# Optimization experiments

Hardware: AMD Instinct MI355X
Metric: run time of the kernel (lower is better)

The kernel has to match this reference:

```python
import jax, jax.numpy as jnp
import numpy as np

B, N, M, D = 64, 197, 65, 768


def setup_inputs() -> dict:
    key = jax.random.key(0)
    k1, k2, k3 = jax.random.split(key, 3)
    image = jax.random.normal(k1, (B, N, D), dtype=jnp.float32)
    text = jax.random.normal(k2, (B, M, D), dtype=jnp.float32)
    pm = jax.random.randint(k3, (B, M), 0, 2).astype(jnp.int32)
    pm = pm.at[:, :2].set(0)  # CLS + first real token always valid
    logit_scale = jnp.ones((), dtype=jnp.float32)
    return {"image": image, "text": text, "padding_masks": pm, "logit_scale": logit_scale}


def _ce_with_diag_labels(logits):
    # F.cross_entropy(logits, arange(B)): mean of -log_softmax diag
    return -jnp.mean(jnp.diagonal(jax.nn.log_softmax(logits, axis=-1)))


def reference(image, text, padding_masks, logit_scale):
    # include_cls_token=False: original computes full [B,B,N,M] then slices
    # [:, :, 1:, 1:]; we compute the sliced tokens directly (same math).
    img = image[:, 1:, :]                   # [B, N-1, D]
    txt = text[:, 1:, :]                    # [B, M-1, D]
    pm = padding_masks[:, 1:].astype(bool)  # [B, M-1] True = padded

    # sim[i,j,n,m] = logit_scale * <img_i,n , txt_j,m>
    sim = logit_scale * jnp.einsum('ind,jmd->ijnm', img, txt)  # [B,B,N-1,M-1]

    # Original masks with NaN along mask of batch-row i (broadcast over j,n).
    # logits_per_image: nan_to_num(-inf) -> max over m -> mean over n
    sim_img = jnp.where(pm[:, None, None, :], -jnp.inf, sim)
    logits_per_image = jnp.mean(jnp.max(sim_img, axis=3), axis=2)  # [B,B]

    # logits_per_text: max over n (NaN cols stay NaN) -> nanmean over m.
    # Equivalent masked mean over valid m (mask constant along n).
    max_n = jnp.max(sim, axis=2)                         # [B,B,M-1]
    valid = ~pm                                          # [B,M-1]
    cnt = jnp.sum(valid, axis=1).astype(sim.dtype)       # [B]
    logits_per_text = jnp.sum(
        jnp.where(valid[:, None, :], max_n, 0.0), axis=2
    ) / cnt[:, None]                                     # [B,B]

    loss = 0.5 * (_ce_with_diag_labels(logits_per_image)
                  + _ce_with_diag_labels(logits_per_text))
    targets = jnp.arange(logits_per_image.shape[0], dtype=jnp.int32)
    return loss, logits_per_image, logits_per_text, targets
```

## Files before the change

### kernel.cpp

```cpp
#include <hip/hip_runtime.h>

typedef _Float16 half8 __attribute__((ext_vector_type(8)));
typedef float floatx4 __attribute__((ext_vector_type(4)));
typedef float float4v __attribute__((ext_vector_type(4)));

#define DIM   768
#define NROW  196
#define AUNITS (64 * 13 * 24 * 64)
#define TUNITS (64 * 4 * 24 * 64)
#define A_HALFS ((size_t)AUNITS * 8)
#define BJ_HALFS (24 * 4 * 64 * 8)

__device__ __forceinline__ void gl_lds16(const _Float16* g, _Float16* l) {
  __builtin_amdgcn_global_load_lds(
      (const __attribute__((address_space(1))) unsigned int*)g,
      (__attribute__((address_space(3))) unsigned int*)l, 16, 0, 0);
}

__global__ __launch_bounds__(256) void repack(const float* __restrict__ img,
                                              const float* __restrict__ txt,
                                              _Float16* __restrict__ Apk,
                                              _Float16* __restrict__ Bpk) {
  int gid = blockIdx.x * 256 + threadIdx.x;
  const float* src;
  _Float16* dst;
  if (gid < AUNITS) {
    int l = gid & 63, g = gid >> 6;
    int s = g % 24; g /= 24;
    int tau = g % 13; int i = g / 13;
    int n = tau * 16 + (l & 15); if (n > 195) n = 195;
    src = img + (size_t)i * 197 * 768 + (size_t)(n + 1) * 768 + s * 32 + (l >> 4) * 8;
    dst = Apk + (size_t)gid * 8;
  } else {
    int u = gid - AUNITS;
    int l = u & 63, g = u >> 6;
    int ct = g & 3; g >>= 2;
    int s = g % 24; int j = g / 24;
    int m = ct * 16 + (l & 15);
    src = txt + (size_t)j * 65 * 768 + (size_t)(m + 1) * 768 + s * 32 + (l >> 4) * 8;
    dst = Bpk + (size_t)u * 8;
  }
  float4v v0 = *(const float4v*)src;
  float4v v1 = *(const float4v*)(src + 4);
  half8 h;
  h[0] = (_Float16)v0[0]; h[1] = (_Float16)v0[1]; h[2] = (_Float16)v0[2]; h[3] = (_Float16)v0[3];
  h[4] = (_Float16)v1[0]; h[5] = (_Float16)v1[1]; h[6] = (_Float16)v1[2]; h[7] = (_Float16)v1[3];
  *(half8*)dst = h;
}

__global__ __launch_bounds__(256, 3) void sim_kernel(const _Float16* __restrict__ Apk,
                                                     const _Float16* __restrict__ Bpk,
                                                     const int* __restrict__ pm,
                                                     const float* __restrict__ ls,
                                                     float* __restrict__ lpi,
                                                     float* __restrict__ lpt) {
  __shared__ _Float16 Bsh[24576];
  __shared__ float colmaxLDS[4][64];
  __shared__ float t12buf[4][64];
  __shared__ float wsumLDS[4];

  const int j = blockIdx.x, i = blockIdx.y;
  const int tid = threadIdx.x;
  const int wave = tid >> 6, lane = tid & 63;
  const int r16 = lane & 15;
  const int lane8 = lane * 8;

  const _Float16* Ai = Apk + (size_t)i * 13 * 24 * 512;
  const _Float16* pA[4];
  pA[0] = Ai + (size_t)(wave)     * 24 * 512 + lane8;
  pA[1] = Ai + (size_t)(wave + 4) * 24 * 512 + lane8;
  pA[2] = Ai + (size_t)(wave + 8) * 24 * 512 + lane8;
  pA[3] = Ai + (size_t)12         * 24 * 512 + lane8;
  const _Float16* Bg = Bpk + (size_t)j * BJ_HALFS;

  half8 af[2][4];
#pragma unroll
  for (int t = 0; t < 4; ++t) {
    af[0][t] = *(const half8*)(pA[t]);
    af[1][t] = *(const half8*)(pA[t] + 512);
  }

  floatx4 acc[3][4];
  floatx4 acc12 = (floatx4){0.f, 0.f, 0.f, 0.f};
#pragma unroll
  for (int t = 0; t < 3; ++t)
#pragma unroll
    for (int cc = 0; cc < 4; ++cc)
      acc[t][cc] = (floatx4){0.f, 0.f, 0.f, 0.f};

  for (int h = 0; h < 2; ++h) {
    __syncthreads();
#pragma unroll
    for (int r = 0; r < 12; ++r) {
      int u = wave * 12 + r;
      gl_lds16(Bg + h * 24576 + u * 512 + lane8, Bsh + u * 512);
    }
    __syncthreads();

#pragma unroll
    for (int sc = 0; sc < 12; ++sc) {
      half8 bfr[4];
#pragma unroll
      for (int cc = 0; cc < 4; ++cc) {
        int ct = (wave + cc) & 3;
        bfr[cc] = *(const half8*)(Bsh + (sc * 4 + ct) * 512 + lane8);
      }
      half8 a0 = af[sc & 1][0], a1 = af[sc & 1][1], a2 = af[sc & 1][2], a3 = af[sc & 1][3];
      if (h == 0 || sc < 10) {
        int s2 = h * 12 + sc + 2;
#pragma unroll
        for (int t = 0; t < 4; ++t) af[sc & 1][t] = *(const half8*)(pA[t] + s2 * 512);
      }
#pragma unroll
      for (int cc = 0; cc < 4; ++cc) {
        acc[0][cc] = __builtin_amdgcn_mfma_f32_16x16x32_f16(a0, bfr[cc], acc[0][cc], 0, 0, 0);
        acc[1][cc] = __builtin_amdgcn_mfma_f32_16x16x32_f16(a1, bfr[cc], acc[1][cc], 0, 0, 0);
        acc[2][cc] = __builtin_amdgcn_mfma_f32_16x16x32_f16(a2, bfr[cc], acc[2][cc], 0, 0, 0);
      }
      acc12 = __builtin_amdgcn_mfma_f32_16x16x32_f16(a3, bfr[0], acc12, 0, 0, 0);
    }
  }

  const float sgl = ls[0];
  bool msk[4];
  int colc[4];
#pragma unroll
  for (int cc = 0; cc < 4; ++cc) {
    colc[cc] = ((wave + cc) & 3) * 16 + r16;
    msk[cc] = pm[i * 65 + 1 + colc[cc]] != 0;
  }

  float rowsum = 0.f;
#pragma unroll
  for (int t = 0; t < 3; ++t) {
#pragma unroll
    for (int r = 0; r < 4; ++r) {
      float rm = -__builtin_inff();
#pragma unroll
      for (int cc = 0; cc < 4; ++cc) {
        float v = acc[t][cc][r] * sgl;
        rm = fmaxf(rm, msk[cc] ? -__builtin_inff() : v);
      }
#pragma unroll
      for (int off = 1; off < 16; off <<= 1)
        rm = fmaxf(rm, __shfl_xor(rm, off, 64));
      rowsum += rm;
    }
  }
#pragma unroll
  for (int off = 1; off < 64; off <<= 1) rowsum += __shfl_xor(rowsum, off, 64);
  if (lane == 0) wsumLDS[wave] = rowsum;

#pragma unroll
  for (int cc = 0; cc < 4; ++cc) {
    float cm = -__builtin_inff();
#pragma unroll
    for (int t = 0; t < 3; ++t)
#pragma unroll
      for (int r = 0; r < 4; ++r)
        cm = fmaxf(cm, acc[t][cc][r] * sgl);
    cm = fmaxf(cm, __shfl_xor(cm, 16, 64));
    cm = fmaxf(cm, __shfl_xor(cm, 32, 64));
    if (lane < 16) colmaxLDS[wave][colc[cc]] = cm;
  }
  if (lane < 16) {
#pragma unroll
    for (int r = 0; r < 4; ++r) t12buf[r][wave * 16 + r16] = acc12[r] * sgl;
  }
  __syncthreads();

  if (tid < 64) {
    int col = tid;
    bool valid = pm[i * 65 + 1 + col] == 0;
    float t0 = t12buf[0][col], t1 = t12buf[1][col], t2 = t12buf[2][col], t3 = t12buf[3][col];
    float v = fmaxf(fmaxf(colmaxLDS[0][col], colmaxLDS[1][col]),
                    fmaxf(colmaxLDS[2][col], colmaxLDS[3][col]));
    v = fmaxf(v, fmaxf(fmaxf(t0, t1), fmaxf(t2, t3)));
    float contrib = valid ? v : 0.f;
    float cntv = valid ? 1.f : 0.f;
    float rs0 = valid ? t0 : -__builtin_inff();
    float rs1 = valid ? t1 : -__builtin_inff();
    float rs2 = valid ? t2 : -__builtin_inff();
    float rs3 = valid ? t3 : -__builtin_inff();
#pragma unroll
    for (int off = 1; off < 64; off <<= 1) {
      contrib += __shfl_xor(contrib, off, 64);
      cntv += __shfl_xor(cntv, off, 64);
      rs0 = fmaxf(rs0, __shfl_xor(rs0, off, 64));
      rs1 = fmaxf(rs1, __shfl_xor(rs1, off, 64));
      rs2 = fmaxf(rs2, __shfl_xor(rs2, off, 64));
      rs3 = fmaxf(rs3, __shfl_xor(rs3, off, 64));
    }
    if (tid == 0) {
      lpt[i * 64 + j] = contrib / cntv;
      float total = (wsumLDS[0] + wsumLDS[1] + wsumLDS[2] + wsumLDS[3]) * 0.0625f
                  + rs0 + rs1 + rs2 + rs3;
      lpi[i * 64 + j] = total / 196.f;
    }
  }
}

__global__ __launch_bounds__(64) void ce_kernel(float* __restrict__ out) {
  const int t = threadIdx.x;
  const float* lpi = out + 1;
  const float* lpt = out + 1 + 4096;

  float mx = -__builtin_inff();
  for (int jj = 0; jj < 64; ++jj) mx = fmaxf(mx, lpi[t * 64 + jj]);
  float se = 0.f;
  for (int jj = 0; jj < 64; ++jj) se += __expf(lpi[t * 64 + jj] - mx);
  float ci = (mx + __logf(se)) - lpi[t * 64 + t];

  float mx2 = -__builtin_inff();
  for (int jj = 0; jj < 64; ++jj) mx2 = fmaxf(mx2, lpt[t * 64 + jj]);
  float se2 = 0.f;
  for (int jj = 0; jj < 64; ++jj) se2 += __expf(lpt[t * 64 + jj] - mx2);
  float ct_ = (mx2 + __logf(se2)) - lpt[t * 64 + t];

  float v = ci + ct_;
#pragma unroll
  for (int off = 1; off < 64; off <<= 1) v += __shfl_xor(v, off, 64);
  if (t == 0) out[0] = 0.5f * v / 64.f;
  out[1 + 8192 + t] = (float)t;
}

extern "C" void kernel_launch(void* const* d_in, const int* in_sizes, int n_in,
                              void* d_out, int out_size, void* d_ws, size_t ws_size,
                              hipStream_t stream) {
  const float* image = (const float*)d_in[0];
  const float* text  = (const float*)d_in[1];
  const int*   pm    = (const int*)d_in[2];
  const float* ls    = (const float*)d_in[3];
  float* out = (float*)d_out;

  _Float16* Apk = (_Float16*)d_ws;
  _Float16* Bpk = Apk + A_HALFS;

  repack<<<(AUNITS + TUNITS) / 256, 256, 0, stream>>>(image, text, Apk, Bpk);

  dim3 grid(64, 64);
  sim_kernel<<<grid, 256, 0, stream>>>(Apk, Bpk, pm, ls, out + 1, out + 1 + 4096);
  ce_kernel<<<1, 64, 0, stream>>>(out);
}
```

Measured before the change: 203.1 us.

## Double-buffer B chunks in LDS and fuse CE loss via last-block atomic

Replaces the two large synchronous B loads with six smaller chunks that are double-buffered, so the next chunk's global-to-LDS load overlaps the MFMA work on the current one. The A prefetch depth grows from two to three steps. Shrinking LDS to 32KB allows the launch bound to ask for four blocks per CU instead of three, with the epilogue scratch reusing the B buffer. The separate cross-entropy kernel is folded into the sim kernel through an atomic counter, so the last block to finish computes the loss; this saves a launch but adds a fence and an atomic in every block.

```diff
diff --git a/kernel.cpp b/kernel.cpp
--- a/kernel.cpp
+++ b/kernel.cpp
@@ -9,7 +9,9 @@
 #define AUNITS (64 * 13 * 24 * 64)
 #define TUNITS (64 * 4 * 24 * 64)
 #define A_HALFS ((size_t)AUNITS * 8)
+#define T_HALFS ((size_t)TUNITS * 8)
 #define BJ_HALFS (24 * 4 * 64 * 8)
+#define CHUNK_H 8192
 
 __device__ __forceinline__ void gl_lds16(const _Float16* g, _Float16* l) {
   __builtin_amdgcn_global_load_lds(
@@ -20,8 +22,10 @@
 __global__ __launch_bounds__(256) void repack(const float* __restrict__ img,
                                               const float* __restrict__ txt,
                                               _Float16* __restrict__ Apk,
-                                              _Float16* __restrict__ Bpk) {
+                                              _Float16* __restrict__ Bpk,
+                                              int* __restrict__ ctr) {
   int gid = blockIdx.x * 256 + threadIdx.x;
+  if (gid == 0) *ctr = 0;
   const float* src;
   _Float16* dst;
   if (gid < AUNITS) {
@@ -48,16 +52,17 @@
   *(half8*)dst = h;
 }
 
-__global__ __launch_bounds__(256, 3) void sim_kernel(const _Float16* __restrict__ Apk,
+__global__ __launch_bounds__(256, 4) void sim_kernel(const _Float16* __restrict__ Apk,
                                                      const _Float16* __restrict__ Bpk,
                                                      const int* __restrict__ pm,
                                                      const float* __restrict__ ls,
-                                                     float* __restrict__ lpi,
-                                                     float* __restrict__ lpt) {
-  __shared__ _Float16 Bsh[24576];
-  __shared__ float colmaxLDS[4][64];
-  __shared__ float t12buf[4][64];
-  __shared__ float wsumLDS[4];
+                                                     float* __restrict__ out,
+                                                     int* __restrict__ ctr) {
+  __shared__ _Float16 Bsh[2 * CHUNK_H];
+  __shared__ int lastFlag;
+
+  float* lpi = out + 1;
+  float* lpt = out + 1 + 4096;
 
   const int j = blockIdx.x, i = blockIdx.y;
   const int tid = threadIdx.x;
@@ -73,12 +78,18 @@
   pA[3] = Ai + (size_t)12         * 24 * 512 + lane8;
   const _Float16* Bg = Bpk + (size_t)j * BJ_HALFS;
 
-  half8 af[2][4];
-#pragma unroll
-  for (int t = 0; t < 4; ++t) {
-    af[0][t] = *(const half8*)(pA[t]);
-    af[1][t] = *(const half8*)(pA[t] + 512);
-  }
+#pragma unroll
+  for (int r = 0; r < 4; ++r) {
+    int u = wave * 4 + r;
+    gl_lds16(Bg + u * 512 + lane8, Bsh + u * 512);
+  }
+
+  half8 af[3][4];
+#pragma unroll
+  for (int d = 0; d < 3; ++d)
+#pragma unroll
+    for (int t = 0; t < 4; ++t)
+      af[d][t] = *(const half8*)(pA[t] + d * 512);
 
   floatx4 acc[3][4];
   floatx4 acc12 = (floatx4){0.f, 0.f, 0.f, 0.f};
@@ -88,28 +99,30 @@
     for (int cc = 0; cc < 4; ++cc)
       acc[t][cc] = (floatx4){0.f, 0.f, 0.f, 0.f};
 
-  for (int h = 0; h < 2; ++h) {
+#pragma unroll
+  for (int c = 0; c < 6; ++c) {
     __syncthreads();
-#pragma unroll
-    for (int r = 0; r < 12; ++r) {
-      int u = wave * 12 + r;
-      gl_lds16(Bg + h * 24576 + u * 512 + lane8, Bsh + u * 512);
-    }
-    __syncthreads();
-
-#pragma unroll
-    for (int sc = 0; sc < 12; ++sc) {
+    if (c < 5) {
+#pragma unroll
+      for (int r = 0; r < 4; ++r) {
+        int u = wave * 4 + r;
+        gl_lds16(Bg + (c + 1) * CHUNK_H + u * 512 + lane8,
+                 Bsh + ((c + 1) & 1) * CHUNK_H + u * 512);
+      }
+    }
+#pragma unroll
+    for (int sc = 0; sc < 4; ++sc) {
+      const int s = c * 4 + sc;
       half8 bfr[4];
 #pragma unroll
       for (int cc = 0; cc < 4; ++cc) {
         int ct = (wave + cc) & 3;
-        bfr[cc] = *(const half8*)(Bsh + (sc * 4 + ct) * 512 + lane8);
-      }
-      half8 a0 = af[sc & 1][0], a1 = af[sc & 1][1], a2 = af[sc & 1][2], a3 = af[sc & 1][3];
-      if (h == 0 || sc < 10) {
-        int s2 = h * 12 + sc + 2;
-#pragma unroll
-        for (int t = 0; t < 4; ++t) af[sc & 1][t] = *(const half8*)(pA[t] + s2 * 512);
+        bfr[cc] = *(const half8*)(Bsh + (c & 1) * CHUNK_H + (sc * 4 + ct) * 512 + lane8);
+      }
+      half8 a0 = af[s % 3][0], a1 = af[s % 3][1], a2 = af[s % 3][2], a3 = af[s % 3][3];
+      if (s < 21) {
+#pragma unroll
+        for (int t = 0; t < 4; ++t) af[s % 3][t] = *(const half8*)(pA[t] + (s + 3) * 512);
       }
 #pragma unroll
       for (int cc = 0; cc < 4; ++cc) {
@@ -149,8 +162,8 @@
   }
 #pragma unroll
   for (int off = 1; off < 64; off <<= 1) rowsum += __shfl_xor(rowsum, off, 64);
-  if (lane == 0) wsumLDS[wave] = rowsum;
-
+
+  float cmv[4];
 #pragma unroll
   for (int cc = 0; cc < 4; ++cc) {
     float cm = -__builtin_inff();
@@ -161,20 +174,29 @@
         cm = fmaxf(cm, acc[t][cc][r] * sgl);
     cm = fmaxf(cm, __shfl_xor(cm, 16, 64));
     cm = fmaxf(cm, __shfl_xor(cm, 32, 64));
-    if (lane < 16) colmaxLDS[wave][colc[cc]] = cm;
-  }
+    cmv[cc] = cm;
+  }
+
+  __syncthreads();
+  float* colmaxLDS = (float*)Bsh;
+  float* t12buf    = (float*)Bsh + 256;
+  float* wsumLDS   = (float*)Bsh + 512;
+
+  if (lane == 0) wsumLDS[wave] = rowsum;
   if (lane < 16) {
 #pragma unroll
-    for (int r = 0; r < 4; ++r) t12buf[r][wave * 16 + r16] = acc12[r] * sgl;
+    for (int cc = 0; cc < 4; ++cc) colmaxLDS[wave * 64 + colc[cc]] = cmv[cc];
+#pragma unroll
+    for (int r = 0; r < 4; ++r) t12buf[r * 64 + wave * 16 + r16] = acc12[r] * sgl;
   }
   __syncthreads();
 
   if (tid < 64) {
     int col = tid;
     bool valid = pm[i * 65 + 1 + col] == 0;
-    float t0 = t12buf[0][col], t1 = t12buf[1][col], t2 = t12buf[2][col], t3 = t12buf[3][col];
-    float v = fmaxf(fmaxf(colmaxLDS[0][col], colmaxLDS[1][col]),
-                    fmaxf(colmaxLDS[2][col], colmaxLDS[3][col]));
+    float t0 = t12buf[col], t1 = t12buf[64 + col], t2 = t12buf[128 + col], t3 = t12buf[192 + col];
+    float v = fmaxf(fmaxf(colmaxLDS[col], colmaxLDS[64 + col]),
+                    fmaxf(colmaxLDS[128 + col], colmaxLDS[192 + col]));
     v = fmaxf(v, fmaxf(fmaxf(t0, t1), fmaxf(t2, t3)));
     float contrib = valid ? v : 0.f;
     float cntv = valid ? 1.f : 0.f;
@@ -193,35 +215,38 @@
     }
     if (tid == 0) {
       lpt[i * 64 + j] = contrib / cntv;
-      float total = (wsumLDS[0] + wsumLDS[1] + wsumLDS[2] + wsumLDS[3]) * 0.0625f
-                  + rs0 + rs1 + rs2 + rs3;
-      lpi[i * 64 + j] = total / 196.f;
-    }
-  }
-}
-
-__global__ __launch_bounds__(64) void ce_kernel(float* __restrict__ out) {
-  const int t = threadIdx.x;
-  const float* lpi = out + 1;
-  const float* lpt = out + 1 + 4096;
-
-  float mx = -__builtin_inff();
-  for (int jj = 0; jj < 64; ++jj) mx = fmaxf(mx, lpi[t * 64 + jj]);
-  float se = 0.f;
-  for (int jj = 0; jj < 64; ++jj) se += __expf(lpi[t * 64 + jj] - mx);
-  float ci = (mx + __logf(se)) - lpi[t * 64 + t];
-
-  float mx2 = -__builtin_inff();
-  for (int jj = 0; jj < 64; ++jj) mx2 = fmaxf(mx2, lpt[t * 64 + jj]);
-  float se2 = 0.f;
-  for (int jj = 0; jj < 64; ++jj) se2 += __expf(lpt[t * 64 + jj] - mx2);
-  float ct_ = (mx2 + __logf(se2)) - lpt[t * 64 + t];
-
-  float v = ci + ct_;
-#pragma unroll
-  for (int off = 1; off < 64; off <<= 1) v += __shfl_xor(v, off, 64);
-  if (t == 0) out[0] = 0.5f * v / 64.f;
-  out[1 + 8192 + t] = (float)t;
+      float wtot = wsumLDS[0] + wsumLDS[1] + wsumLDS[2] + wsumLDS[3];
+      lpi[i * 64 + j] = (wtot * 0.0625f + rs0 + rs1 + rs2 + rs3) / 196.f;
+    }
+  }
+
+  if (tid == 0) {
+    __threadfence();
+    int old = atomicAdd(ctr, 1);
+    lastFlag = (old == 4095);
+  }
+  __syncthreads();
+  if (lastFlag && tid < 64) {
+    __threadfence();
+    const int t = tid;
+    float mx = -__builtin_inff();
+    for (int jj = 0; jj < 64; ++jj) mx = fmaxf(mx, lpi[t * 64 + jj]);
+    float se = 0.f;
+    for (int jj = 0; jj < 64; ++jj) se += __expf(lpi[t * 64 + jj] - mx);
+    float ci = (mx + __logf(se)) - lpi[t * 64 + t];
+
+    float mx2 = -__builtin_inff();
+    for (int jj = 0; jj < 64; ++jj) mx2 = fmaxf(mx2, lpt[t * 64 + jj]);
+    float se2 = 0.f;
+    for (int jj = 0; jj < 64; ++jj) se2 += __expf(lpt[t * 64 + jj] - mx2);
+    float ct_ = (mx2 + __logf(se2)) - lpt[t * 64 + t];
+
+    float v = ci + ct_;
+#pragma unroll
+    for (int off = 1; off < 64; off <<= 1) v += __shfl_xor(v, off, 64);
+    if (t == 0) out[0] = 0.5f * v / 64.f;
+    out[1 + 8192 + t] = (float)t;
+  }
 }
 
 extern "C" void kernel_launch(void* const* d_in, const int* in_sizes, int n_in,
@@ -235,10 +260,10 @@
 
   _Float16* Apk = (_Float16*)d_ws;
   _Float16* Bpk = Apk + A_HALFS;
-
-  repack<<<(AUNITS + TUNITS) / 256, 256, 0, stream>>>(image, text, Apk, Bpk);
+  int* ctr = (int*)(Bpk + T_HALFS);
+
+  repack<<<(AUNITS + TUNITS) / 256, 256, 0, stream>>>(image, text, Apk, Bpk, ctr);
 
   dim3 grid(64, 64);
-  sim_kernel<<<grid, 256, 0, stream>>>(Apk, Bpk, pm, ls, out + 1, out + 1 + 4096);
-  ce_kernel<<<1, 64, 0, stream>>>(out);
-}
+  sim_kernel<<<grid, 256, 0, stream>>>(Apk, Bpk, pm, ls, out, ctr);
+}
```

After: 424.4 us. 109% more time.

## Load B fragments directly from global into registers, dropping LDS staging

Applied to the files above, without the earlier changes.

Removes the shared-memory staging of the text (B) tile and its two block-wide barriers. Each wave now loads its B fragments straight from global memory into registers, double-buffered two k-steps ahead like the A fragments, and the k loop is flattened into 24 unrolled steps. This cuts LDS use and sync stalls, which may allow more occupancy. The cost is that each wave re-fetches B from global/L2 (4x redundant across waves) and register pressure rises.

```diff
diff --git a/kernel.cpp b/kernel.cpp
--- a/kernel.cpp
+++ b/kernel.cpp
@@ -10,12 +10,6 @@
 #define TUNITS (64 * 4 * 24 * 64)
 #define A_HALFS ((size_t)AUNITS * 8)
 #define BJ_HALFS (24 * 4 * 64 * 8)
-
-__device__ __forceinline__ void gl_lds16(const _Float16* g, _Float16* l) {
-  __builtin_amdgcn_global_load_lds(
-      (const __attribute__((address_space(1))) unsigned int*)g,
-      (__attribute__((address_space(3))) unsigned int*)l, 16, 0, 0);
-}
 
 __global__ __launch_bounds__(256) void repack(const float* __restrict__ img,
                                               const float* __restrict__ txt,
@@ -54,7 +48,6 @@
                                                      const float* __restrict__ ls,
                                                      float* __restrict__ lpi,
                                                      float* __restrict__ lpt) {
-  __shared__ _Float16 Bsh[24576];
   __shared__ float colmaxLDS[4][64];
   __shared__ float t12buf[4][64];
   __shared__ float wsumLDS[4];
@@ -71,13 +64,19 @@
   pA[1] = Ai + (size_t)(wave + 4) * 24 * 512 + lane8;
   pA[2] = Ai + (size_t)(wave + 8) * 24 * 512 + lane8;
   pA[3] = Ai + (size_t)12         * 24 * 512 + lane8;
-  const _Float16* Bg = Bpk + (size_t)j * BJ_HALFS;
-
-  half8 af[2][4];
-#pragma unroll
-  for (int t = 0; t < 4; ++t) {
-    af[0][t] = *(const half8*)(pA[t]);
-    af[1][t] = *(const half8*)(pA[t] + 512);
+  const _Float16* pB = Bpk + (size_t)j * BJ_HALFS + lane8;
+
+  half8 af[2][4], bf[2][4];
+#pragma unroll
+  for (int d = 0; d < 2; ++d) {
+#pragma unroll
+    for (int t = 0; t < 4; ++t)
+      af[d][t] = *(const half8*)(pA[t] + d * 512);
+#pragma unroll
+    for (int cc = 0; cc < 4; ++cc) {
+      int ct = (wave + cc) & 3;
+      bf[d][cc] = *(const half8*)(pB + d * 2048 + ct * 512);
+    }
   }
 
   floatx4 acc[3][4];
@@ -88,37 +87,33 @@
     for (int cc = 0; cc < 4; ++cc)
       acc[t][cc] = (floatx4){0.f, 0.f, 0.f, 0.f};
 
-  for (int h = 0; h < 2; ++h) {
-    __syncthreads();
-#pragma unroll
-    for (int r = 0; r < 12; ++r) {
-      int u = wave * 12 + r;
-      gl_lds16(Bg + h * 24576 + u * 512 + lane8, Bsh + u * 512);
-    }
-    __syncthreads();
-
-#pragma unroll
-    for (int sc = 0; sc < 12; ++sc) {
-      half8 bfr[4];
+#pragma unroll
+  for (int s = 0; s < 24; ++s) {
+    half8 a0 = af[s & 1][0], a1 = af[s & 1][1], a2 = af[s & 1][2], a3 = af[s & 1][3];
+    half8 b0 = bf[s & 1][0], b1 = bf[s & 1][1], b2 = bf[s & 1][2], b3 = bf[s & 1][3];
+    if (s < 22) {
+#pragma unroll
+      for (int t = 0; t < 4; ++t)
+        af[s & 1][t] = *(const half8*)(pA[t] + (s + 2) * 512);
 #pragma unroll
       for (int cc = 0; cc < 4; ++cc) {
         int ct = (wave + cc) & 3;
-        bfr[cc] = *(const half8*)(Bsh + (sc * 4 + ct) * 512 + lane8);
+        bf[s & 1][cc] = *(const half8*)(pB + (s + 2) * 2048 + ct * 512);
       }
-      half8 a0 = af[sc & 1][0], a1 = af[sc & 1][1], a2 = af[sc & 1][2], a3 = af[sc & 1][3];
-      if (h == 0 || sc < 10) {
-        int s2 = h * 12 + sc + 2;
-#pragma unroll
-        for (int t = 0; t < 4; ++t) af[sc & 1][t] = *(const half8*)(pA[t] + s2 * 512);
-      }
-#pragma unroll
-      for (int cc = 0; cc < 4; ++cc) {
-        acc[0][cc] = __builtin_amdgcn_mfma_f32_16x16x32_f16(a0, bfr[cc], acc[0][cc], 0, 0, 0);
-        acc[1][cc] = __builtin_amdgcn_mfma_f32_16x16x32_f16(a1, bfr[cc], acc[1][cc], 0, 0, 0);
-        acc[2][cc] = __builtin_amdgcn_mfma_f32_16x16x32_f16(a2, bfr[cc], acc[2][cc], 0, 0, 0);
-      }
-      acc12 = __builtin_amdgcn_mfma_f32_16x16x32_f16(a3, bfr[0], acc12, 0, 0, 0);
-    }
+    }
+    acc[0][0] = __builtin_amdgcn_mfma_f32_16x16x32_f16(a0, b0, acc[0][0], 0, 0, 0);
+    acc[1][0] = __builtin_amdgcn_mfma_f32_16x16x32_f16(a1, b0, acc[1][0], 0, 0, 0);
+    acc[2][0] = __builtin_amdgcn_mfma_f32_16x16x32_f16(a2, b0, acc[2][0], 0, 0, 0);
+    acc12     = __builtin_amdgcn_mfma_f32_16x16x32_f16(a3, b0, acc12,     0, 0, 0);
+    acc[0][1] = __builtin_amdgcn_mfma_f32_16x16x32_f16(a0, b1, acc[0][1], 0, 0, 0);
+    acc[1][1] = __builtin_amdgcn_mfma_f32_16x16x32_f16(a1, b1, acc[1][1], 0, 0, 0);
+    acc[2][1] = __builtin_amdgcn_mfma_f32_16x16x32_f16(a2, b1, acc[2][1], 0, 0, 0);
+    acc[0][2] = __builtin_amdgcn_mfma_f32_16x16x32_f16(a0, b2, acc[0][2], 0, 0, 0);
+    acc[1][2] = __builtin_amdgcn_mfma_f32_16x16x32_f16(a1, b2, acc[1][2], 0, 0, 0);
+    acc[2][2] = __builtin_amdgcn_mfma_f32_16x16x32_f16(a2, b2, acc[2][2], 0, 0, 0);
+    acc[0][3] = __builtin_amdgcn_mfma_f32_16x16x32_f16(a0, b3, acc[0][3], 0, 0, 0);
+    acc[1][3] = __builtin_amdgcn_mfma_f32_16x16x32_f16(a1, b3, acc[1][3], 0, 0, 0);
+    acc[2][3] = __builtin_amdgcn_mfma_f32_16x16x32_f16(a2, b3, acc[2][3], 0, 0, 0);
   }
 
   const float sgl = ls[0];
@@ -149,8 +144,8 @@
   }
 #pragma unroll
   for (int off = 1; off < 64; off <<= 1) rowsum += __shfl_xor(rowsum, off, 64);
-  if (lane == 0) wsumLDS[wave] = rowsum;
-
+
+  float cmv[4];
 #pragma unroll
   for (int cc = 0; cc < 4; ++cc) {
     float cm = -__builtin_inff();
@@ -161,9 +156,13 @@
         cm = fmaxf(cm, acc[t][cc][r] * sgl);
     cm = fmaxf(cm, __shfl_xor(cm, 16, 64));
     cm = fmaxf(cm, __shfl_xor(cm, 32, 64));
-    if (lane < 16) colmaxLDS[wave][colc[cc]] = cm;
-  }
+    cmv[cc] = cm;
+  }
+
+  if (lane == 0) wsumLDS[wave] = rowsum;
   if (lane < 16) {
+#pragma unroll
+    for (int cc = 0; cc < 4; ++cc) colmaxLDS[wave][colc[cc]] = cmv[cc];
 #pragma unroll
     for (int r = 0; r < 4; ++r) t12buf[r][wave * 16 + r16] = acc12[r] * sgl;
   }
@@ -193,9 +192,8 @@
     }
     if (tid == 0) {
       lpt[i * 64 + j] = contrib / cntv;
-      float total = (wsumLDS[0] + wsumLDS[1] + wsumLDS[2] + wsumLDS[3]) * 0.0625f
-                  + rs0 + rs1 + rs2 + rs3;
-      lpi[i * 64 + j] = total / 196.f;
+      float wtot = wsumLDS[0] + wsumLDS[1] + wsumLDS[2] + wsumLDS[3];
+      lpi[i * 64 + j] = (wtot * 0.0625f + rs0 + rs1 + rs2 + rs3) / 196.f;
     }
   }
 }
```

After: 252.2 us. 24.1% more time.
